# Performance work log

Measured on AMD Instinct MI355X. Metric: run time of the kernel, lower is better.

The kernel has to match this reference:

```python
import jax, jax.numpy as jnp
import numpy as np

N = 200000   # gaussians
M = 10000    # scaffold nodes
K = 16       # skinning knn
T = 40       # time steps
F = 32       # semantic feature dim
MAX_S = 0.1
MIN_S = 0.0
EPS = 1e-8


def _qnorm(q):
    return q / jnp.clip(jnp.linalg.norm(q, axis=-1, keepdims=True), 1e-12)


def q2R(q):
    # quaternion (w, x, y, z) -> rotation matrix, normalizing first (matches q2R in source)
    q = _qnorm(q)
    w, x, y, z = q[..., 0], q[..., 1], q[..., 2], q[..., 3]
    r0 = jnp.stack([1 - 2 * (y * y + z * z), 2 * (x * y - w * z), 2 * (x * z + w * y)], -1)
    r1 = jnp.stack([2 * (x * y + w * z), 1 - 2 * (x * x + z * z), 2 * (y * z - w * x)], -1)
    r2 = jnp.stack([2 * (x * z - w * y), 2 * (y * z + w * x), 1 - 2 * (x * x + y * y)], -1)
    return jnp.stack([r0, r1, r2], -2)


def quat_mul(a, b):
    aw, ax, ay, az = a[..., 0], a[..., 1], a[..., 2], a[..., 3]
    bw, bx, by, bz = b[..., 0], b[..., 1], b[..., 2], b[..., 3]
    return jnp.stack([
        aw * bw - ax * bx - ay * by - az * bz,
        aw * bx + ax * bw + ay * bz - az * by,
        aw * by - ax * bz + ay * bw + az * bx,
        aw * bz + ax * by - ay * bx + az * bw], -1)


def quat_conj(q):
    return q * jnp.array([1.0, -1.0, -1.0, -1.0], q.dtype)


def setup_inputs() -> dict:
    key = jax.random.key(0)
    ks = jax.random.split(key, 13)
    return {
        "gs_xyz": 0.05 * jax.random.normal(ks[0], (N, 3), jnp.float32),
        "gs_rotation": jax.random.normal(ks[1], (N, 4), jnp.float32),
        "gs_scaling": jax.random.normal(ks[2], (N, 3), jnp.float32),
        "gs_opacity": jax.random.normal(ks[3], (N, 1), jnp.float32),
        "feat_dc": jax.random.normal(ks[4], (N, 3), jnp.float32),
        "feat_rest": jax.random.normal(ks[5], (N, 9), jnp.float32),
        "node_xyz": jax.random.normal(ks[6], (T, M, 3), jnp.float32),
        "node_quat": jax.random.normal(ks[7], (T, M, 4), jnp.float32),
        "node_sigma": 0.1 + 0.5 * jax.random.uniform(ks[8], (M, 1), jnp.float32),
        "node_sem": jax.random.normal(ks[9], (M, F), jnp.float32),
        "attach_ind": jax.random.randint(ks[10], (N,), 0, M, jnp.int32),
        "ref_time": jax.random.randint(ks[11], (N,), 0, T, jnp.int32),
        "topo_knn": jax.random.randint(ks[12], (M, K), 0, M, jnp.int32),
        "t": 5,
    }


def reference(gs_xyz, gs_rotation, gs_scaling, gs_opacity, feat_dc, feat_rest,
              node_xyz, node_quat, node_sigma, node_sem,
              attach_ind, ref_time, topo_knn, t):
    # --- per-gaussian activated attributes ---
    s = MIN_S + jax.nn.sigmoid(gs_scaling) * (MAX_S - MIN_S)   # s_act
    o = jax.nn.sigmoid(gs_opacity)                              # o_act
    sph = jnp.concatenate([feat_dc, feat_rest], axis=-1)        # [N, 12], full sph order

    # --- leaf-local -> world at ref time (get_xyz / get_R_mtx) ---
    ref_p_attach = node_xyz[ref_time, attach_ind]               # [N,3] async knn gather
    ref_q_attach = node_quat[ref_time, attach_ind]              # [N,4]
    R_ref_attach = q2R(ref_q_attach)                            # [N,3,3]
    x_world = jnp.einsum('nij,nj->ni', R_ref_attach, gs_xyz) + ref_p_attach
    R_world = jnp.einsum('nij,njk->nik', R_ref_attach, q2R(gs_rotation))

    # --- scf.warp: KNN skinning from per-point ref time to target time t ---
    sk_ind = topo_knn[attach_ind]                               # [N,K] neighbor node ids
    p_ref = node_xyz[ref_time[:, None], sk_ind]                 # [N,K,3]
    q_ref = node_quat[ref_time[:, None], sk_ind]                # [N,K,4]
    p_live = node_xyz[t][sk_ind]                                # [N,K,3]
    q_live = node_quat[t][sk_ind]                               # [N,K,4]
    sigma = node_sigma[sk_ind, 0]                               # [N,K]

    diff = x_world[:, None, :] - p_ref                          # [N,K,3]
    dsq = jnp.sum(diff * diff, axis=-1)                         # [N,K]
    w = jnp.exp(-dsq / (2.0 * sigma * sigma + EPS))             # RBF skinning weights
    w = w / (jnp.sum(w, axis=-1, keepdims=True) + EPS)          # [N,K]

    # per-node relative transform ref -> live
    q_rel = quat_mul(_qnorm(q_live), quat_conj(_qnorm(q_ref)))  # [N,K,4]
    R_rel = q2R(q_rel)                                          # [N,K,3,3]
    mu_k = jnp.einsum('nkij,nkj->nki', R_rel, diff) + p_live    # [N,K,3]
    mu_live = jnp.einsum('nk,nki->ni', w, mu_k)                 # [N,3]

    q_blend = jnp.einsum('nk,nkd->nd', w, q_rel)                # blended quaternion
    fr_live = jnp.einsum('nij,njk->nik', q2R(q_blend), R_world) # [N,3,3]

    sem_live = jnp.einsum('nk,nkf->nf', w, node_sem[sk_ind])    # [N,F]

    return mu_live, fr_live, s, o, sph, sem_live
```

## Files before the change

### kernel.cpp

```cpp
#include <hip/hip_runtime.h>

#define KNN 16
#define FSEM 32
#define LPG 4
#define NXCD 8
#define CSTRIDE 32
#define MAXT 256

__device__ __forceinline__ float sigmoidf_(float x) { return 1.0f / (1.0f + __expf(-x)); }

__device__ __forceinline__ void quat_to_R(float qw, float qx, float qy, float qz, float* R) {
    float d = qw * qw + qx * qx + qy * qy + qz * qz;
    float inv = rsqrtf(fmaxf(d, 1e-24f));
    float w = qw * inv, x = qx * inv, y = qy * inv, z = qz * inv;
    R[0] = 1.f - 2.f * (y * y + z * z); R[1] = 2.f * (x * y - w * z); R[2] = 2.f * (x * z + w * y);
    R[3] = 2.f * (x * y + w * z); R[4] = 1.f - 2.f * (x * x + z * z); R[5] = 2.f * (y * z - w * x);
    R[6] = 2.f * (x * z - w * y); R[7] = 2.f * (y * z + w * x); R[8] = 1.f - 2.f * (x * x + y * y);
}

__global__ void __launch_bounds__(256)
k_pack_hist(const float* __restrict__ node_xyz, const float* __restrict__ node_quat,
            const float* __restrict__ node_sigma,
            const int* __restrict__ rtime,
            float* __restrict__ packed, int* __restrict__ cnt,
            int TM, int M, int N, int T)
{
    __shared__ int lh[MAXT];
    if (threadIdx.x < MAXT) lh[threadIdx.x] = 0;
    __syncthreads();

    const int p = blockIdx.x * blockDim.x + threadIdx.x;
    if (cnt && p < N) atomicAdd(&lh[rtime[p]], 1);

    if (p < TM) {
        const int node = p - (p / M) * M;
        const float* x = node_xyz + 3 * (size_t)p;
        float4 a = make_float4(x[0], x[1], x[2], node_sigma[node]);
        float4 q = reinterpret_cast<const float4*>(node_quat)[p];
        float4* dst = reinterpret_cast<float4*>(packed + 8 * (size_t)p);
        dst[0] = a;
        dst[1] = q;
    }

    __syncthreads();
    if (cnt && threadIdx.x < T) {
        const int c = lh[threadIdx.x];
        if (c > 0) atomicAdd(&cnt[threadIdx.x * CSTRIDE], c);
    }
}

__global__ void __launch_bounds__(256)
k_scatter_elem(const int* __restrict__ attach, const int* __restrict__ rtime,
               const float* __restrict__ gs_xyz,
               const float* __restrict__ gs_rot,
               const int* __restrict__ cnt, int* __restrict__ cur,
               float4* __restrict__ meta,
               const float* __restrict__ gs_scal,
               const float* __restrict__ gs_opa,
               const float* __restrict__ feat_dc,
               const float* __restrict__ feat_rest,
               float* __restrict__ out,
               int N, int T)
{
    __shared__ int lh[MAXT];
    __shared__ int bb[MAXT];
    __shared__ int pref[MAXT];

    if (threadIdx.x < MAXT) lh[threadIdx.x] = 0;
    __syncthreads();

    const int n = blockIdx.x * blockDim.x + threadIdx.x;
    const bool valid = (n < N);
    int a = 0, rt = 0, lrank = 0;
    if (valid) {
        a  = attach[n];
        rt = rtime[n];
        lrank = atomicAdd(&lh[rt], 1);
    }
    __syncthreads();

    if (threadIdx.x < T) {
        const int c = lh[threadIdx.x];
        bb[threadIdx.x] = (c > 0) ? atomicAdd(&cur[threadIdx.x * CSTRIDE], c) : 0;
        pref[threadIdx.x] = cnt[threadIdx.x * CSTRIDE];
    }
    __syncthreads();
    if (threadIdx.x == 0) {
        int run = 0;
#pragma unroll 4
        for (int i = 0; i < T; i++) { const int c = pref[i]; pref[i] = run; run += c; }
    }
    __syncthreads();

    if (!valid) return;

    const int pos = pref[rt] + bb[rt] + lrank;
    meta[3 * (size_t)pos]     = make_float4(__int_as_float(n), 0.f,
                                            __int_as_float(rt), __int_as_float(a));
    meta[3 * (size_t)pos + 1] = make_float4(gs_xyz[3 * (size_t)n + 0],
                                            gs_xyz[3 * (size_t)n + 1],
                                            gs_xyz[3 * (size_t)n + 2], 0.f);
    meta[3 * (size_t)pos + 2] = reinterpret_cast<const float4*>(gs_rot)[n];

    const size_t Ns = (size_t)N, ns = (size_t)n;
    float* os = out + 12 * Ns + 3 * ns;
    os[0] = 0.1f * sigmoidf_(gs_scal[3 * ns + 0]);
    os[1] = 0.1f * sigmoidf_(gs_scal[3 * ns + 1]);
    os[2] = 0.1f * sigmoidf_(gs_scal[3 * ns + 2]);

    out[15 * Ns + ns] = sigmoidf_(gs_opa[ns]);

    float* osph = out + 16 * Ns + 12 * ns;
    float4 v0 = make_float4(feat_dc[3 * ns + 0], feat_dc[3 * ns + 1], feat_dc[3 * ns + 2],
                            feat_rest[9 * ns + 0]);
    float4 v1 = make_float4(feat_rest[9 * ns + 1], feat_rest[9 * ns + 2],
                            feat_rest[9 * ns + 3], feat_rest[9 * ns + 4]);
    float4 v2 = make_float4(feat_rest[9 * ns + 5], feat_rest[9 * ns + 6],
                            feat_rest[9 * ns + 7], feat_rest[9 * ns + 8]);
    reinterpret_cast<float4*>(osph)[0] = v0;
    reinterpret_cast<float4*>(osph)[1] = v1;
    reinterpret_cast<float4*>(osph)[2] = v2;
}

__global__ void __launch_bounds__(256)
k_elem(const float* __restrict__ gs_scal,
       const float* __restrict__ gs_opa,
       const float* __restrict__ feat_dc,
       const float* __restrict__ feat_rest,
       float* __restrict__ out, int N)
{
    const int n = blockIdx.x * blockDim.x + threadIdx.x;
    if (n >= N) return;
    const size_t Ns = (size_t)N, ns = (size_t)n;

    float* os = out + 12 * Ns + 3 * ns;
    os[0] = 0.1f * sigmoidf_(gs_scal[3 * ns + 0]);
    os[1] = 0.1f * sigmoidf_(gs_scal[3 * ns + 1]);
    os[2] = 0.1f * sigmoidf_(gs_scal[3 * ns + 2]);

    out[15 * Ns + ns] = sigmoidf_(gs_opa[ns]);

    float* osph = out + 16 * Ns + 12 * ns;
    float4 v0 = make_float4(feat_dc[3 * ns + 0], feat_dc[3 * ns + 1], feat_dc[3 * ns + 2],
                            feat_rest[9 * ns + 0]);
    float4 v1 = make_float4(feat_rest[9 * ns + 1], feat_rest[9 * ns + 2],
                            feat_rest[9 * ns + 3], feat_rest[9 * ns + 4]);
    float4 v2 = make_float4(feat_rest[9 * ns + 5], feat_rest[9 * ns + 6],
                            feat_rest[9 * ns + 7], feat_rest[9 * ns + 8]);
    reinterpret_cast<float4*>(osph)[0] = v0;
    reinterpret_cast<float4*>(osph)[1] = v1;
    reinterpret_cast<float4*>(osph)[2] = v2;
}

template<bool PACKED, bool SORTED>
__global__ void __launch_bounds__(256)
dynscf_kernel(const float* __restrict__ gs_xyz,
              const float* __restrict__ gs_rot,
              const float* __restrict__ node_xyz,
              const float* __restrict__ node_quat,
              const float* __restrict__ packed,
              const float* __restrict__ node_sigma,
              const float* __restrict__ node_sem,
              const int* __restrict__ attach_ind,
              const int* __restrict__ ref_time,
              const int* __restrict__ topo_knn,
              const int* __restrict__ t_ptr,
              const float4* __restrict__ meta,
              float* __restrict__ out,
              int N, int M)
{
    int bid = blockIdx.x;
    if (SORTED) {
        const int nwg = gridDim.x;
        const int q = nwg / NXCD, r = nwg % NXCD;
        const int xcd = bid % NXCD, idx = bid / NXCD;
        bid = (xcd < r ? xcd * (q + 1) : r * (q + 1) + (xcd - r) * q) + idx;
    }
    const int tid = bid * blockDim.x + threadIdx.x;
    const int g   = tid >> 2;
    const int sub = tid & (LPG - 1);
    if (g >= N) return;

    const int t = t_ptr[0];

    int n, a, rt;
    float gx, gy, gz;
    if (SORTED) {
        const float4 m0 = meta[3 * (size_t)g];
        const float4 m1 = meta[3 * (size_t)g + 1];
        n  = __float_as_int(m0.x);
        rt = __float_as_int(m0.z);
        a  = __float_as_int(m0.w);
        gx = m1.x; gy = m1.y; gz = m1.z;
    } else {
        n  = g;
        a  = attach_ind[n];
        rt = ref_time[n];
        gx = gs_xyz[3 * (size_t)n + 0];
        gy = gs_xyz[3 * (size_t)n + 1];
        gz = gs_xyz[3 * (size_t)n + 2];
    }

    const size_t base_rt = (size_t)rt * (size_t)M;
    const size_t base_t  = (size_t)t  * (size_t)M;

    const int4 kv = reinterpret_cast<const int4*>(topo_knn)[(size_t)a * (KNN / 4) + sub];
    const int js[4] = { kv.x, kv.y, kv.z, kv.w };

    float apx, apy, apz, aqw, aqx, aqy, aqz;
    if (PACKED) {
        const float4* pk = reinterpret_cast<const float4*>(packed + (base_rt + (size_t)a) * 8);
        float4 xz = pk[0], qv = pk[1];
        apx = xz.x; apy = xz.y; apz = xz.z;
        aqw = qv.x; aqx = qv.y; aqy = qv.z; aqz = qv.w;
    } else {
        const float4 qv = *reinterpret_cast<const float4*>(node_quat + (base_rt + (size_t)a) * 4);
        const float* pa = node_xyz + (base_rt + (size_t)a) * 3;
        apx = pa[0]; apy = pa[1]; apz = pa[2];
        aqw = qv.x; aqx = qv.y; aqy = qv.z; aqz = qv.w;
    }
    float xw0, xw1, xw2;
    {
        float Rf[9];
        quat_to_R(aqw, aqx, aqy, aqz, Rf);
        xw0 = Rf[0] * gx + Rf[1] * gy + Rf[2] * gz + apx;
        xw1 = Rf[3] * gx + Rf[4] * gy + Rf[5] * gz + apy;
        xw2 = Rf[6] * gx + Rf[7] * gy + Rf[8] * gz + apz;
    }

    float wsum = 0.f, mu0 = 0.f, mu1 = 0.f, mu2 = 0.f;
    float qb0 = 0.f, qb1 = 0.f, qb2 = 0.f, qb3 = 0.f;
    float wk[4];

#pragma unroll
    for (int k = 0; k < KNN / LPG; k++) {
        const int j = js[k];

        float prx, pry, prz, rw, rx, ry, rz;
        float plx, ply, plz, lw, lx, ly, lz;
        float sg;
        if (PACKED) {
            const float4* pkr = reinterpret_cast<const float4*>(packed + (base_rt + (size_t)j) * 8);
            float4 xr = pkr[0], qr = pkr[1];
            prx = xr.x; pry = xr.y; prz = xr.z; sg = xr.w;
            rw = qr.x; rx = qr.y; ry = qr.z; rz = qr.w;
            const float4* pkl = reinterpret_cast<const float4*>(packed + (base_t + (size_t)j) * 8);
            float4 xl = pkl[0], ql = pkl[1];
            plx = xl.x; ply = xl.y; plz = xl.z;
            lw = ql.x; lx = ql.y; ly = ql.z; lz = ql.w;
        } else {
            const float* pr = node_xyz + (base_rt + (size_t)j) * 3;
            prx = pr[0]; pry = pr[1]; prz = pr[2];
            const float4 qr = *reinterpret_cast<const float4*>(node_quat + (base_rt + (size_t)j) * 4);
            rw = qr.x; rx = qr.y; ry = qr.z; rz = qr.w;
            const float* pl = node_xyz + (base_t + (size_t)j) * 3;
            plx = pl[0]; ply = pl[1]; plz = pl[2];
            const float4 ql = *reinterpret_cast<const float4*>(node_quat + (base_t + (size_t)j) * 4);
            lw = ql.x; lx = ql.y; ly = ql.z; lz = ql.w;
            sg = node_sigma[j];
        }

        const float dx = xw0 - prx;
        const float dy = xw1 - pry;
        const float dz = xw2 - prz;
        const float dsq = dx * dx + dy * dy + dz * dz;

        const float w = __expf(-dsq / (2.f * sg * sg + 1e-8f));
        wk[k] = w;

        {
            float inv = rsqrtf(fmaxf(rw * rw + rx * rx + ry * ry + rz * rz, 1e-24f));
            rw *= inv; rx *= inv; ry *= inv; rz *= inv;
        }
        {
            float inv = rsqrtf(fmaxf(lw * lw + lx * lx + ly * ly + lz * lz, 1e-24f));
            lw *= inv; lx *= inv; ly *= inv; lz *= inv;
        }
        const float qw =  lw * rw + lx * rx + ly * ry + lz * rz;
        const float qx = -lw * rx + lx * rw - ly * rz + lz * ry;
        const float qy = -lw * ry + lx * rz + ly * rw - lz * rx;
        const float qz = -lw * rz - lx * ry + ly * rx + lz * rw;

        float Rr[9];
        quat_to_R(qw, qx, qy, qz, Rr);

        const float m0 = Rr[0] * dx + Rr[1] * dy + Rr[2] * dz + plx;
        const float m1 = Rr[3] * dx + Rr[4] * dy + Rr[5] * dz + ply;
        const float m2 = Rr[6] * dx + Rr[7] * dy + Rr[8] * dz + plz;

        wsum += w;
        mu0 += w * m0; mu1 += w * m1; mu2 += w * m2;
        qb0 += w * qw; qb1 += w * qx; qb2 += w * qy; qb3 += w * qz;
    }

#pragma unroll
    for (int m = 1; m < LPG; m <<= 1) {
        wsum += __shfl_xor(wsum, m);
        mu0  += __shfl_xor(mu0, m);  mu1 += __shfl_xor(mu1, m);  mu2 += __shfl_xor(mu2, m);
        qb0  += __shfl_xor(qb0, m);  qb1 += __shfl_xor(qb1, m);
        qb2  += __shfl_xor(qb2, m);  qb3 += __shfl_xor(qb3, m);
    }

    const float invw = 1.f / (wsum + 1e-8f);
    const size_t Ns = (size_t)N, ns = (size_t)n;

    float sm0 = 0.f, sm1 = 0.f, sm2 = 0.f, sm3 = 0.f;
    float sm4 = 0.f, sm5 = 0.f, sm6 = 0.f, sm7 = 0.f;
    const float4* sem4 = reinterpret_cast<const float4*>(node_sem);
#pragma unroll
    for (int kk = 0; kk < KNN; kk++) {
        const int src = kk >> 2;
        const int idx = kk & 3;
        const int   jk = __shfl(js[idx], src, LPG);
        const float wkk = __shfl(wk[idx], src, LPG);
        const float4 v0 = sem4[(size_t)jk * (FSEM / 4) + sub * 2 + 0];
        const float4 v1 = sem4[(size_t)jk * (FSEM / 4) + sub * 2 + 1];
        sm0 += wkk * v0.x; sm1 += wkk * v0.y; sm2 += wkk * v0.z; sm3 += wkk * v0.w;
        sm4 += wkk * v1.x; sm5 += wkk * v1.y; sm6 += wkk * v1.z; sm7 += wkk * v1.w;
    }

    if (sub == 0) {
        out[3 * ns + 0] = mu0 * invw;
        out[3 * ns + 1] = mu1 * invw;
        out[3 * ns + 2] = mu2 * invw;
    } else if (sub == 1) {
        float4 qg;
        if (SORTED) qg = meta[3 * (size_t)g + 2];
        else        qg = *reinterpret_cast<const float4*>(gs_rot + 4 * ns);
        float Rref[9];
        quat_to_R(aqw, aqx, aqy, aqz, Rref);
        float Rg[9];
        quat_to_R(qg.x, qg.y, qg.z, qg.w, Rg);
        float Rw[9];
#pragma unroll
        for (int i = 0; i < 3; i++)
#pragma unroll
            for (int j = 0; j < 3; j++)
                Rw[3 * i + j] = Rref[3 * i] * Rg[j] + Rref[3 * i + 1] * Rg[3 + j] + Rref[3 * i + 2] * Rg[6 + j];
        float Rb[9];
        quat_to_R(qb0 * invw, qb1 * invw, qb2 * invw, qb3 * invw, Rb);
        float* ofr = out + 3 * Ns + 9 * ns;
#pragma unroll
        for (int i = 0; i < 3; i++)
#pragma unroll
            for (int j = 0; j < 3; j++)
                ofr[3 * i + j] = Rb[3 * i] * Rw[j] + Rb[3 * i + 1] * Rw[3 + j] + Rb[3 * i + 2] * Rw[6 + j];
    }

    float4* osem = reinterpret_cast<float4*>(out + 28 * Ns + FSEM * ns);
    osem[sub * 2 + 0] = make_float4(sm0 * invw, sm1 * invw, sm2 * invw, sm3 * invw);
    osem[sub * 2 + 1] = make_float4(sm4 * invw, sm5 * invw, sm6 * invw, sm7 * invw);
}

extern "C" void kernel_launch(void* const* d_in, const int* in_sizes, int n_in,
                              void* d_out, int out_size, void* d_ws, size_t ws_size,
                              hipStream_t stream)
{
    const float* gs_xyz     = (const float*)d_in[0];
    const float* gs_rot     = (const float*)d_in[1];
    const float* gs_scal    = (const float*)d_in[2];
    const float* gs_opa     = (const float*)d_in[3];
    const float* feat_dc    = (const float*)d_in[4];
    const float* feat_rest  = (const float*)d_in[5];
    const float* node_xyz   = (const float*)d_in[6];
    const float* node_quat  = (const float*)d_in[7];
    const float* node_sigma = (const float*)d_in[8];
    const float* node_sem   = (const float*)d_in[9];
    const int* attach_ind   = (const int*)d_in[10];
    const int* ref_time     = (const int*)d_in[11];
    const int* topo_knn     = (const int*)d_in[12];
    const int* t_ptr        = (const int*)d_in[13];

    const int N = in_sizes[0] / 3;
    const int M = in_sizes[8];
    const int TM = in_sizes[6] / 3;
    const int T  = TM / M;

    float* out = (float*)d_out;

    const int block = 256;
    const int gridN = (N + block - 1) / block;
    const long long threads = (long long)N * LPG;
    const int gridM = (int)((threads + block - 1) / block);
    const int gridPH = (((TM > N ? TM : N)) + block - 1) / block;

    const size_t f_packed = (size_t)TM * 8;
    const size_t f_meta   = (size_t)N * 12;
    const size_t i_cnt    = (size_t)MAXT * CSTRIDE;
    const size_t i_cur    = (size_t)MAXT * CSTRIDE;
    const size_t need_sort   = (f_packed + f_meta + i_cnt + i_cur) * sizeof(float);
    const size_t need_packed = f_packed * sizeof(float);

    if (ws_size >= need_sort && T <= MAXT) {
        float*  packed = (float*)d_ws;
        float4* meta   = (float4*)(packed + f_packed);
        int*    cnt    = (int*)(packed + f_packed + f_meta);
        int*    cur    = cnt + i_cnt;

        hipMemsetAsync(cnt, 0, (i_cnt + i_cur) * sizeof(int), stream);
        hipLaunchKernelGGL(k_pack_hist, dim3(gridPH), dim3(block), 0, stream,
                           node_xyz, node_quat, node_sigma, ref_time,
                           packed, cnt, TM, M, N, T);
        hipLaunchKernelGGL(k_scatter_elem, dim3(gridN), dim3(block), 0, stream,
                           attach_ind, ref_time, gs_xyz, gs_rot, cnt, cur, meta,
                           gs_scal, gs_opa, feat_dc, feat_rest, out, N, T);
        hipLaunchKernelGGL((dynscf_kernel<true, true>), dim3(gridM), dim3(block), 0, stream,
                           gs_xyz, gs_rot, node_xyz, node_quat, packed, node_sigma, node_sem,
                           attach_ind, ref_time, topo_knn, t_ptr, meta, out, N, M);
    } else if (ws_size >= need_packed) {
        float* packed = (float*)d_ws;
        hipLaunchKernelGGL(k_pack_hist, dim3(gridPH), dim3(block), 0, stream,
                           node_xyz, node_quat, node_sigma, ref_time,
                           packed, (int*)nullptr, TM, M, 0, T);
        hipLaunchKernelGGL((dynscf_kernel<true, false>), dim3(gridM), dim3(block), 0, stream,
                           gs_xyz, gs_rot, node_xyz, node_quat, packed, node_sigma, node_sem,
                           attach_ind, ref_time, topo_knn, t_ptr, (const float4*)nullptr,
                           out, N, M);
        hipLaunchKernelGGL(k_elem, dim3(gridN), dim3(block), 0, stream,
                           gs_scal, gs_opa, feat_dc, feat_rest, out, N);
    } else {
        hipLaunchKernelGGL((dynscf_kernel<false, false>), dim3(gridM), dim3(block), 0, stream,
                           gs_xyz, gs_rot, node_xyz, node_quat, (const float*)nullptr,
                           node_sigma, node_sem,
                           attach_ind, ref_time, topo_knn, t_ptr, (const float4*)nullptr,
                           out, N, M);
        hipLaunchKernelGGL(k_elem, dim3(gridN), dim3(block), 0, stream,
                           gs_scal, gs_opa, feat_dc, feat_rest, out, N);
    }
}
```

Baseline: 212.2 us.

## Sort gaussians by (ref_time, attach node) with a cooperative prep kernel

Replaces the memset, histogram and scatter kernels with one cooperative kernel. It counting-sorts gaussians by the full (ref_time, attach) key using grid-wide syncs and a two-level prefix scan. The metadata record shrinks from three float4s to two, and the rotation goes into its own array. Finer sorting should improve gather locality for the attach node's knn in the main kernel, at the cost of grid syncs, global atomics on 400k counters, and a serial block-0 scan. Falls back to the old path if the cooperative launch fails.

Result: slower. 522.0 us (+146.0%).

```diff
diff --git a/kernel.cpp b/kernel.cpp
--- a/kernel.cpp
+++ b/kernel.cpp
@@ -1,4 +1,7 @@
 #include <hip/hip_runtime.h>
+#include <hip/hip_cooperative_groups.h>
+
+namespace cg = cooperative_groups;
 
 #define KNN 16
 #define FSEM 32
@@ -18,90 +21,13 @@
     R[6] = 2.f * (x * z - w * y); R[7] = 2.f * (y * z + w * x); R[8] = 1.f - 2.f * (x * x + y * y);
 }
 
-__global__ void __launch_bounds__(256)
-k_pack_hist(const float* __restrict__ node_xyz, const float* __restrict__ node_quat,
-            const float* __restrict__ node_sigma,
-            const int* __restrict__ rtime,
-            float* __restrict__ packed, int* __restrict__ cnt,
-            int TM, int M, int N, int T)
-{
-    __shared__ int lh[MAXT];
-    if (threadIdx.x < MAXT) lh[threadIdx.x] = 0;
-    __syncthreads();
-
-    const int p = blockIdx.x * blockDim.x + threadIdx.x;
-    if (cnt && p < N) atomicAdd(&lh[rtime[p]], 1);
-
-    if (p < TM) {
-        const int node = p - (p / M) * M;
-        const float* x = node_xyz + 3 * (size_t)p;
-        float4 a = make_float4(x[0], x[1], x[2], node_sigma[node]);
-        float4 q = reinterpret_cast<const float4*>(node_quat)[p];
-        float4* dst = reinterpret_cast<float4*>(packed + 8 * (size_t)p);
-        dst[0] = a;
-        dst[1] = q;
-    }
-
-    __syncthreads();
-    if (cnt && threadIdx.x < T) {
-        const int c = lh[threadIdx.x];
-        if (c > 0) atomicAdd(&cnt[threadIdx.x * CSTRIDE], c);
-    }
-}
-
-__global__ void __launch_bounds__(256)
-k_scatter_elem(const int* __restrict__ attach, const int* __restrict__ rtime,
-               const float* __restrict__ gs_xyz,
-               const float* __restrict__ gs_rot,
-               const int* __restrict__ cnt, int* __restrict__ cur,
-               float4* __restrict__ meta,
-               const float* __restrict__ gs_scal,
-               const float* __restrict__ gs_opa,
-               const float* __restrict__ feat_dc,
-               const float* __restrict__ feat_rest,
-               float* __restrict__ out,
-               int N, int T)
-{
-    __shared__ int lh[MAXT];
-    __shared__ int bb[MAXT];
-    __shared__ int pref[MAXT];
-
-    if (threadIdx.x < MAXT) lh[threadIdx.x] = 0;
-    __syncthreads();
-
-    const int n = blockIdx.x * blockDim.x + threadIdx.x;
-    const bool valid = (n < N);
-    int a = 0, rt = 0, lrank = 0;
-    if (valid) {
-        a  = attach[n];
-        rt = rtime[n];
-        lrank = atomicAdd(&lh[rt], 1);
-    }
-    __syncthreads();
-
-    if (threadIdx.x < T) {
-        const int c = lh[threadIdx.x];
-        bb[threadIdx.x] = (c > 0) ? atomicAdd(&cur[threadIdx.x * CSTRIDE], c) : 0;
-        pref[threadIdx.x] = cnt[threadIdx.x * CSTRIDE];
-    }
-    __syncthreads();
-    if (threadIdx.x == 0) {
-        int run = 0;
-#pragma unroll 4
-        for (int i = 0; i < T; i++) { const int c = pref[i]; pref[i] = run; run += c; }
-    }
-    __syncthreads();
-
-    if (!valid) return;
-
-    const int pos = pref[rt] + bb[rt] + lrank;
-    meta[3 * (size_t)pos]     = make_float4(__int_as_float(n), 0.f,
-                                            __int_as_float(rt), __int_as_float(a));
-    meta[3 * (size_t)pos + 1] = make_float4(gs_xyz[3 * (size_t)n + 0],
-                                            gs_xyz[3 * (size_t)n + 1],
-                                            gs_xyz[3 * (size_t)n + 2], 0.f);
-    meta[3 * (size_t)pos + 2] = reinterpret_cast<const float4*>(gs_rot)[n];
-
+__device__ __forceinline__ void elem_outputs(int n, int N,
+                                             const float* __restrict__ gs_scal,
+                                             const float* __restrict__ gs_opa,
+                                             const float* __restrict__ feat_dc,
+                                             const float* __restrict__ feat_rest,
+                                             float* __restrict__ out)
+{
     const size_t Ns = (size_t)N, ns = (size_t)n;
     float* os = out + 12 * Ns + 3 * ns;
     os[0] = 0.1f * sigmoidf_(gs_scal[3 * ns + 0]);
@@ -123,6 +49,194 @@
 }
 
 __global__ void __launch_bounds__(256)
+k_prep(const float* __restrict__ node_xyz, const float* __restrict__ node_quat,
+       const float* __restrict__ node_sigma,
+       const int* __restrict__ attach, const int* __restrict__ rtime,
+       const float* __restrict__ gs_xyz, const float* __restrict__ gs_rot,
+       const float* __restrict__ gs_scal, const float* __restrict__ gs_opa,
+       const float* __restrict__ feat_dc, const float* __restrict__ feat_rest,
+       float* __restrict__ packed,
+       int* __restrict__ cnt, int* __restrict__ blk,
+       float4* __restrict__ metaA, float4* __restrict__ rotA,
+       float* __restrict__ out,
+       int TM, int M, int N, int B, int nchunk)
+{
+    cg::grid_group grid = cg::this_grid();
+    const int gsize = gridDim.x * blockDim.x;
+    const int gtid  = blockIdx.x * blockDim.x + threadIdx.x;
+    __shared__ int sh[256];
+
+    for (int i = gtid; i < B; i += gsize) cnt[i] = 0;
+    grid.sync();
+
+    const int PMAX = (TM > N) ? TM : N;
+    for (int p = gtid; p < PMAX; p += gsize) {
+        if (p < TM) {
+            const int node = p - (p / M) * M;
+            const float* x = node_xyz + 3 * (size_t)p;
+            float4 axyz = make_float4(x[0], x[1], x[2], node_sigma[node]);
+            float4 q = reinterpret_cast<const float4*>(node_quat)[p];
+            float4* dst = reinterpret_cast<float4*>(packed + 8 * (size_t)p);
+            dst[0] = axyz;
+            dst[1] = q;
+        }
+        if (p < N) {
+            const int key = rtime[p] * M + attach[p];
+            atomicAdd(&cnt[key], 1);
+        }
+    }
+    grid.sync();
+
+    for (int c = blockIdx.x; c < nchunk; c += gridDim.x) {
+        const int i = c * 256 + threadIdx.x;
+        int v = (i < B) ? cnt[i] : 0;
+        sh[threadIdx.x] = v;
+        __syncthreads();
+        int acc = v;
+#pragma unroll
+        for (int off = 1; off < 256; off <<= 1) {
+            int u = (threadIdx.x >= off) ? sh[threadIdx.x - off] : 0;
+            __syncthreads();
+            acc += u;
+            sh[threadIdx.x] = acc;
+            __syncthreads();
+        }
+        if (i < B) cnt[i] = acc - v;
+        if (threadIdx.x == 255) blk[c] = acc;
+        __syncthreads();
+    }
+    grid.sync();
+
+    if (blockIdx.x == 0) {
+        __shared__ int carry_s;
+        if (threadIdx.x == 0) carry_s = 0;
+        __syncthreads();
+        for (int base = 0; base < nchunk; base += 256) {
+            const int i = base + threadIdx.x;
+            int v = (i < nchunk) ? blk[i] : 0;
+            sh[threadIdx.x] = v;
+            __syncthreads();
+            int acc = v;
+#pragma unroll
+            for (int off = 1; off < 256; off <<= 1) {
+                int u = (threadIdx.x >= off) ? sh[threadIdx.x - off] : 0;
+                __syncthreads();
+                acc += u;
+                sh[threadIdx.x] = acc;
+                __syncthreads();
+            }
+            const int carry = carry_s;
+            if (i < nchunk) blk[i] = acc - v + carry;
+            __syncthreads();
+            if (threadIdx.x == 255) carry_s = carry + acc;
+            __syncthreads();
+        }
+    }
+    grid.sync();
+
+    for (int n = gtid; n < N; n += gsize) {
+        const int a = attach[n], rt = rtime[n];
+        const int key = rt * M + a;
+        const int pos = atomicAdd(&cnt[key], 1) + blk[key >> 8];
+        metaA[2 * (size_t)pos]     = make_float4(__int_as_float(n), __int_as_float(a),
+                                                 __int_as_float(rt), 0.f);
+        metaA[2 * (size_t)pos + 1] = make_float4(gs_xyz[3 * (size_t)n + 0],
+                                                 gs_xyz[3 * (size_t)n + 1],
+                                                 gs_xyz[3 * (size_t)n + 2], 0.f);
+        rotA[pos] = reinterpret_cast<const float4*>(gs_rot)[n];
+
+        elem_outputs(n, N, gs_scal, gs_opa, feat_dc, feat_rest, out);
+    }
+}
+
+__global__ void __launch_bounds__(256)
+k_pack_hist(const float* __restrict__ node_xyz, const float* __restrict__ node_quat,
+            const float* __restrict__ node_sigma,
+            const int* __restrict__ rtime,
+            float* __restrict__ packed, int* __restrict__ cnt,
+            int TM, int M, int N, int T)
+{
+    __shared__ int lh[MAXT];
+    if (threadIdx.x < MAXT) lh[threadIdx.x] = 0;
+    __syncthreads();
+
+    const int p = blockIdx.x * blockDim.x + threadIdx.x;
+    if (cnt && p < N) atomicAdd(&lh[rtime[p]], 1);
+
+    if (p < TM) {
+        const int node = p - (p / M) * M;
+        const float* x = node_xyz + 3 * (size_t)p;
+        float4 a = make_float4(x[0], x[1], x[2], node_sigma[node]);
+        float4 q = reinterpret_cast<const float4*>(node_quat)[p];
+        float4* dst = reinterpret_cast<float4*>(packed + 8 * (size_t)p);
+        dst[0] = a;
+        dst[1] = q;
+    }
+
+    __syncthreads();
+    if (cnt && threadIdx.x < T) {
+        const int c = lh[threadIdx.x];
+        if (c > 0) atomicAdd(&cnt[threadIdx.x * CSTRIDE], c);
+    }
+}
+
+__global__ void __launch_bounds__(256)
+k_scatter_elem(const int* __restrict__ attach, const int* __restrict__ rtime,
+               const float* __restrict__ gs_xyz,
+               const float* __restrict__ gs_rot,
+               const int* __restrict__ cnt, int* __restrict__ cur,
+               float4* __restrict__ metaA, float4* __restrict__ rotA,
+               const float* __restrict__ gs_scal,
+               const float* __restrict__ gs_opa,
+               const float* __restrict__ feat_dc,
+               const float* __restrict__ feat_rest,
+               float* __restrict__ out,
+               int N, int T)
+{
+    __shared__ int lh[MAXT];
+    __shared__ int bb[MAXT];
+    __shared__ int pref[MAXT];
+
+    if (threadIdx.x < MAXT) lh[threadIdx.x] = 0;
+    __syncthreads();
+
+    const int n = blockIdx.x * blockDim.x + threadIdx.x;
+    const bool valid = (n < N);
+    int a = 0, rt = 0, lrank = 0;
+    if (valid) {
+        a  = attach[n];
+        rt = rtime[n];
+        lrank = atomicAdd(&lh[rt], 1);
+    }
+    __syncthreads();
+
+    if (threadIdx.x < T) {
+        const int c = lh[threadIdx.x];
+        bb[threadIdx.x] = (c > 0) ? atomicAdd(&cur[threadIdx.x * CSTRIDE], c) : 0;
+        pref[threadIdx.x] = cnt[threadIdx.x * CSTRIDE];
+    }
+    __syncthreads();
+    if (threadIdx.x == 0) {
+        int run = 0;
+#pragma unroll 4
+        for (int i = 0; i < T; i++) { const int c = pref[i]; pref[i] = run; run += c; }
+    }
+    __syncthreads();
+
+    if (!valid) return;
+
+    const int pos = pref[rt] + bb[rt] + lrank;
+    metaA[2 * (size_t)pos]     = make_float4(__int_as_float(n), __int_as_float(a),
+                                             __int_as_float(rt), 0.f);
+    metaA[2 * (size_t)pos + 1] = make_float4(gs_xyz[3 * (size_t)n + 0],
+                                             gs_xyz[3 * (size_t)n + 1],
+                                             gs_xyz[3 * (size_t)n + 2], 0.f);
+    rotA[pos] = reinterpret_cast<const float4*>(gs_rot)[n];
+
+    elem_outputs(n, N, gs_scal, gs_opa, feat_dc, feat_rest, out);
+}
+
+__global__ void __launch_bounds__(256)
 k_elem(const float* __restrict__ gs_scal,
        const float* __restrict__ gs_opa,
        const float* __restrict__ feat_dc,
@@ -131,25 +245,7 @@
 {
     const int n = blockIdx.x * blockDim.x + threadIdx.x;
     if (n >= N) return;
-    const size_t Ns = (size_t)N, ns = (size_t)n;
-
-    float* os = out + 12 * Ns + 3 * ns;
-    os[0] = 0.1f * sigmoidf_(gs_scal[3 * ns + 0]);
-    os[1] = 0.1f * sigmoidf_(gs_scal[3 * ns + 1]);
-    os[2] = 0.1f * sigmoidf_(gs_scal[3 * ns + 2]);
-
-    out[15 * Ns + ns] = sigmoidf_(gs_opa[ns]);
-
-    float* osph = out + 16 * Ns + 12 * ns;
-    float4 v0 = make_float4(feat_dc[3 * ns + 0], feat_dc[3 * ns + 1], feat_dc[3 * ns + 2],
-                            feat_rest[9 * ns + 0]);
-    float4 v1 = make_float4(feat_rest[9 * ns + 1], feat_rest[9 * ns + 2],
-                            feat_rest[9 * ns + 3], feat_rest[9 * ns + 4]);
-    float4 v2 = make_float4(feat_rest[9 * ns + 5], feat_rest[9 * ns + 6],
-                            feat_rest[9 * ns + 7], feat_rest[9 * ns + 8]);
-    reinterpret_cast<float4*>(osph)[0] = v0;
-    reinterpret_cast<float4*>(osph)[1] = v1;
-    reinterpret_cast<float4*>(osph)[2] = v2;
+    elem_outputs(n, N, gs_scal, gs_opa, feat_dc, feat_rest, out);
 }
 
 template<bool PACKED, bool SORTED>
@@ -165,7 +261,8 @@
               const int* __restrict__ ref_time,
               const int* __restrict__ topo_knn,
               const int* __restrict__ t_ptr,
-              const float4* __restrict__ meta,
+              const float4* __restrict__ metaA,
+              const float4* __restrict__ rotA,
               float* __restrict__ out,
               int N, int M)
 {
@@ -186,11 +283,11 @@
     int n, a, rt;
     float gx, gy, gz;
     if (SORTED) {
-        const float4 m0 = meta[3 * (size_t)g];
-        const float4 m1 = meta[3 * (size_t)g + 1];
+        const float4 m0 = metaA[2 * (size_t)g];
+        const float4 m1 = metaA[2 * (size_t)g + 1];
         n  = __float_as_int(m0.x);
+        a  = __float_as_int(m0.y);
         rt = __float_as_int(m0.z);
-        a  = __float_as_int(m0.w);
         gx = m1.x; gy = m1.y; gz = m1.z;
     } else {
         n  = g;
@@ -325,7 +422,7 @@
         out[3 * ns + 2] = mu2 * invw;
     } else if (sub == 1) {
         float4 qg;
-        if (SORTED) qg = meta[3 * (size_t)g + 2];
+        if (SORTED) qg = rotA[g];
         else        qg = *reinterpret_cast<const float4*>(gs_rot + 4 * ns);
         float Rref[9];
         quat_to_R(aqw, aqx, aqy, aqz, Rref);
@@ -375,6 +472,8 @@
     const int M = in_sizes[8];
     const int TM = in_sizes[6] / 3;
     const int T  = TM / M;
+    const int B  = TM;
+    const int nchunk = (B + 255) / 256;
 
     float* out = (float*)d_out;
 
@@ -385,28 +484,66 @@
     const int gridPH = (((TM > N ? TM : N)) + block - 1) / block;
 
     const size_t f_packed = (size_t)TM * 8;
-    const size_t f_meta   = (size_t)N * 12;
-    const size_t i_cnt    = (size_t)MAXT * CSTRIDE;
-    const size_t i_cur    = (size_t)MAXT * CSTRIDE;
-    const size_t need_sort   = (f_packed + f_meta + i_cnt + i_cur) * sizeof(float);
+    const size_t f_meta   = (size_t)N * 8;
+    const size_t f_rot    = (size_t)N * 4;
+    const size_t i_cnt    = (size_t)B;
+    const size_t i_blk    = 2048;
+    const size_t need_sort   = (f_packed + f_meta + f_rot + i_cnt + i_blk) * sizeof(float);
     const size_t need_packed = f_packed * sizeof(float);
 
-    if (ws_size >= need_sort && T <= MAXT) {
+    if (ws_size >= need_sort && T <= MAXT && nchunk <= 2048) {
         float*  packed = (float*)d_ws;
-        float4* meta   = (float4*)(packed + f_packed);
-        int*    cnt    = (int*)(packed + f_packed + f_meta);
-        int*    cur    = cnt + i_cnt;
-
-        hipMemsetAsync(cnt, 0, (i_cnt + i_cur) * sizeof(int), stream);
-        hipLaunchKernelGGL(k_pack_hist, dim3(gridPH), dim3(block), 0, stream,
-                           node_xyz, node_quat, node_sigma, ref_time,
-                           packed, cnt, TM, M, N, T);
-        hipLaunchKernelGGL(k_scatter_elem, dim3(gridN), dim3(block), 0, stream,
-                           attach_ind, ref_time, gs_xyz, gs_rot, cnt, cur, meta,
-                           gs_scal, gs_opa, feat_dc, feat_rest, out, N, T);
+        float4* metaA  = (float4*)(packed + f_packed);
+        float4* rotA   = (float4*)(packed + f_packed + f_meta);
+        int*    cnt    = (int*)(packed + f_packed + f_meta + f_rot);
+        int*    blk    = cnt + i_cnt;
+
+        static int coopBlocks = -1;
+        if (coopBlocks < 0) {
+            int nb = 0;
+            hipError_t oe = hipOccupancyMaxActiveBlocksPerMultiprocessor(&nb, k_prep, 256, 0);
+            int cus = 256;
+            hipDeviceProp_t prop;
+            if (hipGetDeviceProperties(&prop, 0) == hipSuccess && prop.multiProcessorCount > 0)
+                cus = prop.multiProcessorCount;
+            coopBlocks = (oe == hipSuccess && nb > 0) ? nb * cus : 0;
+        }
+
+        bool coop_ok = false;
+        if (coopBlocks > 0) {
+            int G = gridPH < coopBlocks ? gridPH : coopBlocks;
+            if (G < 1) G = 1;
+            void* args[] = {
+                (void*)&node_xyz, (void*)&node_quat, (void*)&node_sigma,
+                (void*)&attach_ind, (void*)&ref_time,
+                (void*)&gs_xyz, (void*)&gs_rot, (void*)&gs_scal, (void*)&gs_opa,
+                (void*)&feat_dc, (void*)&feat_rest,
+                (void*)&packed, (void*)&cnt, (void*)&blk,
+                (void*)&metaA, (void*)&rotA, (void*)&out,
+                (void*)&TM, (void*)&M, (void*)&N, (void*)&B, (void*)&nchunk
+            };
+            hipError_t err = hipLaunchCooperativeKernel(
+                reinterpret_cast<const void*>(&k_prep), dim3(G), dim3(block),
+                args, 0u, stream);
+            coop_ok = (err == hipSuccess);
+        }
+
+        if (!coop_ok) {
+            int* cntF = cnt;
+            int* curF = cnt + MAXT * CSTRIDE;
+            hipMemsetAsync(cntF, 0, (size_t)2 * MAXT * CSTRIDE * sizeof(int), stream);
+            hipLaunchKernelGGL(k_pack_hist, dim3(gridPH), dim3(block), 0, stream,
+                               node_xyz, node_quat, node_sigma, ref_time,
+                               packed, cntF, TM, M, N, T);
+            hipLaunchKernelGGL(k_scatter_elem, dim3(gridN), dim3(block), 0, stream,
+                               attach_ind, ref_time, gs_xyz, gs_rot, cntF, curF,
+                               metaA, rotA, gs_scal, gs_opa, feat_dc, feat_rest,
+                               out, N, T);
+        }
+
         hipLaunchKernelGGL((dynscf_kernel<true, true>), dim3(gridM), dim3(block), 0, stream,
                            gs_xyz, gs_rot, node_xyz, node_quat, packed, node_sigma, node_sem,
-                           attach_ind, ref_time, topo_knn, t_ptr, meta, out, N, M);
+                           attach_ind, ref_time, topo_knn, t_ptr, metaA, rotA, out, N, M);
     } else if (ws_size >= need_packed) {
         float* packed = (float*)d_ws;
         hipLaunchKernelGGL(k_pack_hist, dim3(gridPH), dim3(block), 0, stream,
@@ -414,16 +551,16 @@
                            packed, (int*)nullptr, TM, M, 0, T);
         hipLaunchKernelGGL((dynscf_kernel<true, false>), dim3(gridM), dim3(block), 0, stream,
                            gs_xyz, gs_rot, node_xyz, node_quat, packed, node_sigma, node_sem,
-                           attach_ind, ref_time, topo_knn, t_ptr, (const float4*)nullptr,
-                           out, N, M);
+                           attach_ind, ref_time, topo_knn, t_ptr,
+                           (const float4*)nullptr, (const float4*)nullptr, out, N, M);
         hipLaunchKernelGGL(k_elem, dim3(gridN), dim3(block), 0, stream,
                            gs_scal, gs_opa, feat_dc, feat_rest, out, N);
     } else {
         hipLaunchKernelGGL((dynscf_kernel<false, false>), dim3(gridM), dim3(block), 0, stream,
                            gs_xyz, gs_rot, node_xyz, node_quat, (const float*)nullptr,
                            node_sigma, node_sem,
-                           attach_ind, ref_time, topo_knn, t_ptr, (const float4*)nullptr,
-                           out, N, M);
+                           attach_ind, ref_time, topo_knn, t_ptr,
+                           (const float4*)nullptr, (const float4*)nullptr, out, N, M);
         hipLaunchKernelGGL(k_elem, dim3(gridN), dim3(block), 0, stream,
                            gs_scal, gs_opa, feat_dc, feat_rest, out, N);
     }
```
